# Kernel tuning notes

Measured on AMD Instinct MI355X. Metric: run time of the kernel, lower is better.

## Reference

```python
import jax, jax.numpy as jnp
import numpy as np

D_MODEL, N, L_MAX, BATCH = 512, 64, 2048, 8


def _make_s4_buffers(n):
    # HiPPO-NPLR: hippo[i,j] = sqrt(2i+1)sqrt(2j+1) if i>j; i+1 if i==j (1-indexed)
    i = np.arange(1, n + 1)
    row = np.sqrt(2 * i + 1.0)
    hippo = np.tril(np.outer(row, row), -1) + np.diag(i + 1.0)
    p = 0.5 * np.sqrt(2 * i + 1.0)
    q = 2.0 * p
    S = -hippo + np.outer(p, q)
    lam, V = np.linalg.eig(S)
    Vc = V.conj().T
    return Vc @ p, Vc @ q, lam  # complex128 -> cast to complex64 later


def setup_inputs() -> dict:
    key = jax.random.key(0)
    k1, k2, k3, k4 = jax.random.split(key, 4)
    xavier_std = float(np.sqrt(2.0 / (N + D_MODEL)))
    p, q, lam = _make_s4_buffers(N)
    u = jax.random.normal(k1, (BATCH, L_MAX, D_MODEL), jnp.float32)
    B = jax.random.normal(k2, (D_MODEL, N), jnp.float32) * xavier_std
    Ct = jax.random.normal(k3, (D_MODEL, N), jnp.float32) * xavier_std
    D = jnp.ones((D_MODEL,), jnp.float32)
    log_step = (jax.random.uniform(k4, (D_MODEL,), jnp.float32)
                * (np.log(0.1) - np.log(0.001)) + np.log(0.001))
    return {
        "u": u, "B": B, "Ct": Ct, "D": D, "log_step": log_step,
        "p": jnp.asarray(p, jnp.complex64),
        "q": jnp.asarray(q, jnp.complex64),
        "lam": jnp.asarray(lam, jnp.complex64),
    }


def _s4_forward(u, B, Ct, D, log_step, p, q, lam):
    L = u.shape[1]  # l_max
    omega = jnp.exp((2j * np.pi / L) * jnp.arange(L)).astype(jnp.complex64)  # (L,)
    step = jnp.exp(log_step)                                                 # (d,)
    g = (2.0 / step)[:, None] * ((1.0 - omega) / (1.0 + omega))[None, :]     # (d, L)
    c = 2.0 / (1.0 + omega)                                                  # (L,)
    Bc = B.astype(jnp.complex64)
    Ctc = Ct.astype(jnp.complex64)  # Ct is real -> conj is identity
    v00 = Ctc * Bc                              # (d, n)
    v01 = Ctc * p[None, :]                      # (d, n)
    v10 = jnp.conj(q)[None, :] * Bc             # (d, n)
    v11 = jnp.broadcast_to(jnp.conj(q) * p, v00.shape)
    V = jnp.stack([v00, v01, v10, v11], 0)      # (4, d, n)
    # fused Cauchy reduction: k[k,d,l] = sum_n V[k,d,n] / (g[d,l] - lam[n])
    recip = 1.0 / (g[:, :, None] - lam[None, None, :])  # (d, L, n) big intermediate
    k00, k01, k10, k11 = jnp.einsum('kdn,dln->kdl', V, recip)
    at_roots = c * (k00 - k01 * k10 / (1.0 + k11))      # (d, L)
    # ifft + index reversal (i -> (L - i) mod L), keep real part
    order = (L - jnp.arange(L)) % L
    K = jnp.fft.ifft(at_roots, n=L, axis=-1)[:, order].real.astype(jnp.float32)  # (d, L)
    # non-circular convolution via length-2L FFT
    ud = jnp.fft.rfft(jnp.pad(u, ((0, 0), (0, L), (0, 0))), axis=1)   # (B, L+1, d)
    Kd = jnp.fft.rfft(jnp.pad(K, ((0, 0), (0, L))), axis=-1)          # (d, L+1)
    y = jnp.fft.irfft(jnp.swapaxes(ud, 1, 2) * Kd[None], axis=-1)[..., :L]  # (B, d, L)
    return jnp.swapaxes(y, 1, 2) + D[None, None, :] * u


def reference(u, B, Ct, D, log_step, p, q, lam):
    return _s4_forward(u, B, Ct, D, log_step, p, q, lam)
```

## Files before the change

kernel.cpp:

```cpp
#include <hip/hip_runtime.h>
#include <math.h>

#define D_MODEL 512
#define NSTATE  64
#define LSEQ    2048
#define L2X     4096
#define NBATCH  8
#define NT      512
#define CNT     256

#define SQ2H 0.70710678118654752f
#define C16  0.92387953251128674f
#define S16  0.38268343236508977f
#define A4096 (-1.5339807878856412e-3f)

__device__ __forceinline__ float2 cmulf(float2 a, float2 b) {
    return make_float2(a.x * b.x - a.y * b.y, a.x * b.y + a.y * b.x);
}
__device__ __forceinline__ float2 cmulc(float2 a, float2 w) {
    return make_float2(a.x * w.x + a.y * w.y, a.y * w.x - a.x * w.y);
}
__device__ __forceinline__ float2 cadd(float2 a, float2 b) { return make_float2(a.x + b.x, a.y + b.y); }
__device__ __forceinline__ float2 csub(float2 a, float2 b) { return make_float2(a.x - b.x, a.y - b.y); }
__device__ __forceinline__ float rcpf(float x) { return __builtin_amdgcn_rcpf(x); }
__device__ __forceinline__ float2 cdiv_fast(float2 a, float2 b) {
    float inv = rcpf(b.x * b.x + b.y * b.y);
    return make_float2((a.x * b.x + a.y * b.y) * inv, (a.y * b.x - a.x * b.y) * inv);
}
__device__ __forceinline__ int finitef(float v) {
    return (v == v) && (v < 3.0e38f) && (v > -3.0e38f);
}
__device__ __forceinline__ int hexrev12(int x) {
    return ((x & 15) << 8) | (x & 240) | ((x >> 8) & 15);
}

__device__ __forceinline__ int tidx(int i) { return i + (i >> 4); }
__device__ __forceinline__ int kswz(int i) { return i ^ (i >> 6); }

#define TW_SZ  1088
#define BUF_SZ 4352

__device__ __forceinline__ float2 twget4(const float2* tw, int k) {
    float2 w = tw[tidx(k & 1023)];
    if (k & 1024) w = make_float2(w.y, -w.x);
    if (k & 2048) w = make_float2(-w.x, -w.y);
    return w;
}
__device__ __forceinline__ void build_tw(float2* tw) {
    for (int k = threadIdx.x; k < 1024; k += NT) {
        float s, c;
        sincosf(A4096 * (float)k, &s, &c);
        tw[tidx(k)] = make_float2(c, s);
    }
}

__device__ __forceinline__ float2 ldc(const float* f, int n, int mode) {
    if (mode == 0) return make_float2(f[n], 0.0f);
    if (mode == 1) return make_float2(f[n], f[64 + n]);
    return make_float2(f[2 * n], f[2 * n + 1]);
}

__device__ __forceinline__ void dft4f(float2 a, float2 b, float2 c, float2 d, float2* F) {
    float2 t0 = cadd(a, c), t1 = csub(a, c);
    float2 t2 = cadd(b, d), t3 = csub(b, d);
    F[0] = cadd(t0, t2);
    F[1] = make_float2(t1.x + t3.y, t1.y - t3.x);
    F[2] = csub(t0, t2);
    F[3] = make_float2(t1.x - t3.y, t1.y + t3.x);
}
__device__ __forceinline__ void dft4i(float2 a, float2 b, float2 c, float2 d, float2* F) {
    float2 t0 = cadd(a, c), t1 = csub(a, c);
    float2 t2 = cadd(b, d), t3 = csub(b, d);
    F[0] = cadd(t0, t2);
    F[1] = make_float2(t1.x - t3.y, t1.y + t3.x);
    F[2] = csub(t0, t2);
    F[3] = make_float2(t1.x + t3.y, t1.y - t3.x);
}
__device__ __forceinline__ void dft8f(const float2* a, float2* X) {
    float2 E[4], O[4];
    dft4f(a[0], a[2], a[4], a[6], E);
    dft4f(a[1], a[3], a[5], a[7], O);
    float2 o1 = make_float2(SQ2H * (O[1].x + O[1].y), SQ2H * (O[1].y - O[1].x));
    float2 o2 = make_float2(O[2].y, -O[2].x);
    float2 o3 = make_float2(SQ2H * (O[3].y - O[3].x), -SQ2H * (O[3].x + O[3].y));
    X[0] = cadd(E[0], O[0]); X[4] = csub(E[0], O[0]);
    X[1] = cadd(E[1], o1);   X[5] = csub(E[1], o1);
    X[2] = cadd(E[2], o2);   X[6] = csub(E[2], o2);
    X[3] = cadd(E[3], o3);   X[7] = csub(E[3], o3);
}
__device__ __forceinline__ void dft8i(const float2* a, float2* X) {
    float2 E[4], O[4];
    dft4i(a[0], a[2], a[4], a[6], E);
    dft4i(a[1], a[3], a[5], a[7], O);
    float2 o1 = make_float2(SQ2H * (O[1].x - O[1].y), SQ2H * (O[1].y + O[1].x));
    float2 o2 = make_float2(-O[2].y, O[2].x);
    float2 o3 = make_float2(-SQ2H * (O[3].x + O[3].y), SQ2H * (O[3].x - O[3].y));
    X[0] = cadd(E[0], O[0]); X[4] = csub(E[0], O[0]);
    X[1] = cadd(E[1], o1);   X[5] = csub(E[1], o1);
    X[2] = cadd(E[2], o2);   X[6] = csub(E[2], o2);
    X[3] = cadd(E[3], o3);   X[7] = csub(E[3], o3);
}
__device__ __forceinline__ void dft16f(const float2* a, float2* X) {
    float2 ev[8], od[8], E[8], O[8];
    #pragma unroll
    for (int r = 0; r < 8; r++) { ev[r] = a[2 * r]; od[r] = a[2 * r + 1]; }
    dft8f(ev, E); dft8f(od, O);
    float2 t0 = O[0];
    float2 t1 = cmulf(O[1], make_float2(C16, -S16));
    float2 t2 = make_float2(SQ2H * (O[2].x + O[2].y), SQ2H * (O[2].y - O[2].x));
    float2 t3 = cmulf(O[3], make_float2(S16, -C16));
    float2 t4 = make_float2(O[4].y, -O[4].x);
    float2 t5 = cmulf(O[5], make_float2(-S16, -C16));
    float2 t6 = make_float2(SQ2H * (O[6].y - O[6].x), -SQ2H * (O[6].x + O[6].y));
    float2 t7 = cmulf(O[7], make_float2(-C16, -S16));
    X[0] = cadd(E[0], t0); X[8]  = csub(E[0], t0);
    X[1] = cadd(E[1], t1); X[9]  = csub(E[1], t1);
    X[2] = cadd(E[2], t2); X[10] = csub(E[2], t2);
    X[3] = cadd(E[3], t3); X[11] = csub(E[3], t3);
    X[4] = cadd(E[4], t4); X[12] = csub(E[4], t4);
    X[5] = cadd(E[5], t5); X[13] = csub(E[5], t5);
    X[6] = cadd(E[6], t6); X[14] = csub(E[6], t6);
    X[7] = cadd(E[7], t7); X[15] = csub(E[7], t7);
}
__device__ __forceinline__ void dft16i(const float2* a, float2* X) {
    float2 ev[8], od[8], E[8], O[8];
    #pragma unroll
    for (int r = 0; r < 8; r++) { ev[r] = a[2 * r]; od[r] = a[2 * r + 1]; }
    dft8i(ev, E); dft8i(od, O);
    float2 t0 = O[0];
    float2 t1 = cmulf(O[1], make_float2(C16, S16));
    float2 t2 = make_float2(SQ2H * (O[2].x - O[2].y), SQ2H * (O[2].x + O[2].y));
    float2 t3 = cmulf(O[3], make_float2(S16, C16));
    float2 t4 = make_float2(-O[4].y, O[4].x);
    float2 t5 = cmulf(O[5], make_float2(-S16, C16));
    float2 t6 = make_float2(-SQ2H * (O[6].x + O[6].y), SQ2H * (O[6].x - O[6].y));
    float2 t7 = cmulf(O[7], make_float2(-C16, S16));
    X[0] = cadd(E[0], t0); X[8]  = csub(E[0], t0);
    X[1] = cadd(E[1], t1); X[9]  = csub(E[1], t1);
    X[2] = cadd(E[2], t2); X[10] = csub(E[2], t2);
    X[3] = cadd(E[3], t3); X[11] = csub(E[3], t3);
    X[4] = cadd(E[4], t4); X[12] = csub(E[4], t4);
    X[5] = cadd(E[5], t5); X[13] = csub(E[5], t5);
    X[6] = cadd(E[6], t6); X[14] = csub(E[6], t6);
    X[7] = cadd(E[7], t7); X[15] = csub(E[7], t7);
}

template<int H, bool TW>
__device__ __forceinline__ void r16_dif_ld(float2* buf, const float2* twp, int t) {
    const int j = t & (H - 1);
    const int i0 = ((t - j) << 4) + j;
    const int base = i0 + (i0 >> 4);
    constexpr int S = (H >= 16) ? (H + (H >> 4)) : 1;
    float2 a[16], X[16];
    #pragma unroll
    for (int k = 0; k < 16; k++) a[k] = buf[base + k * S];
    dft16f(a, X);
    buf[base] = X[0];
    #pragma unroll
    for (int m = 1; m < 16; m++) {
        float2 v = X[m];
        if (TW) v = cmulf(v, twp[(m - 1) * 16 + j]);
        buf[base + m * S] = v;
    }
}
template<int H, bool TW>
__device__ __forceinline__ void r16_dit_ld(float2* buf, const float2* twp, int t) {
    const int j = t & (H - 1);
    const int i0 = ((t - j) << 4) + j;
    const int base = i0 + (i0 >> 4);
    constexpr int S = (H >= 16) ? (H + (H >> 4)) : 1;
    float2 a[16], X[16];
    a[0] = buf[base];
    #pragma unroll
    for (int k = 1; k < 16; k++) {
        float2 v = buf[base + k * S];
        if (TW) v = cmulc(v, twp[(k - 1) * 16 + j]);
        a[k] = v;
    }
    dft16i(a, X);
    #pragma unroll
    for (int m = 0; m < 16; m++) buf[base + m * S] = X[m];
}

template<int H, int F, int TWMODE, int NBF>
__device__ __forceinline__ void r8_dif_stage(float2* buf, const float2* tw, const float2* twp) {
    __syncthreads();
    const int tid = threadIdx.x;
    if (NBF >= NT || tid < NBF) {
        const int j = tid & (H - 1);
        const int i0 = ((tid - j) << 3) + j;
        float2 a[8], X[8];
        #pragma unroll
        for (int k = 0; k < 8; k++) a[k] = buf[tidx(i0 + k * H)];
        dft8f(a, X);
        if (TWMODE == 1) {
            #pragma unroll
            for (int m = 1; m < 8; m++) X[m] = cmulf(X[m], twp[(m - 1) * H + j]);
        } else if (TWMODE == 2) {
            #pragma unroll
            for (int m = 1; m < 8; m++) X[m] = cmulf(X[m], twget4(tw, (j * F * m) & 4095));
        }
        #pragma unroll
        for (int m = 0; m < 8; m++) buf[tidx(i0 + m * H)] = X[m];
    }
}
__device__ __forceinline__ void r4_dif_h1(float2* buf) {
    __syncthreads();
    const int tid = threadIdx.x;
    const int i0 = tid << 2;
    float2 F[4];
    dft4f(buf[tidx(i0)], buf[tidx(i0 + 1)], buf[tidx(i0 + 2)], buf[tidx(i0 + 3)], F);
    #pragma unroll
    for (int m = 0; m < 4; m++) buf[tidx(i0 + m)] = F[m];
}

__global__ __launch_bounds__(NT) void s4_khat_kernel(
    const float* __restrict__ Bmat, const float* __restrict__ Ct,
    const float* __restrict__ log_step,
    const float* __restrict__ pf, const float* __restrict__ qf,
    const float* __restrict__ lf,
    float2* __restrict__ Khat, int size_hint)
{
    __shared__ float2 tw[TW_SZ];
    __shared__ float2 buf[BUF_SZ];
    __shared__ float2 stash[289];
    __shared__ float2 twK2[224];
    __shared__ float2 twK3[28];
    __shared__ float2 twp2[240];
    const int d = blockIdx.x;
    const int tid = threadIdx.x;

    build_tw(tw);
    if (tid < 224) { int m = (tid >> 5) + 1, j = tid & 31; float s, c;
        sincosf(A4096 * (float)(16 * j * m), &s, &c); twK2[tid] = make_float2(c, s); }
    else if (tid < 252) { int r = tid - 224; int m = (r >> 3) + 1, j = r & 7; float s, c;
        sincosf(A4096 * (float)(128 * j * m), &s, &c); twK3[r] = make_float2(c, s); }
    else if (tid < 492) { int r = tid - 252; int m = (r >> 4) + 1, j = r & 15; float s, c;
        sincosf(A4096 * (float)(16 * j * m), &s, &c); twp2[r] = make_float2(c, s); }

    int mode;
    if (size_hint >= 128) {
        mode = (fabsf(lf[1] + 0.5f) < 0.05f) ? 1 : 2;
    } else {
        float s1 = 0.0f, s2 = 0.0f;
        bool ok = true;
        for (int n = 0; n < 64; n++) {
            float v = lf[64 + n];
            if (!finitef(v)) { ok = false; break; }
            s1 += v; s2 += fabsf(v);
        }
        mode = (ok && s2 > 0.5f && s2 < 1.0e6f && fabsf(s1) < 1.0e-2f * s2) ? 1 : 0;
    }

    float2* v01  = stash;
    float2* v10  = stash + 64;
    float2* v11  = stash + 128;
    float2* lamS = stash + 192;
    float*  v00  = (float*)(stash + 256);

    if (tid < NSTATE) {
        int n = tid;
        float Bdn = Bmat[d * NSTATE + n];
        float Cdn = Ct[d * NSTATE + n];
        float2 pn = ldc(pf, n, mode);
        float2 qn = ldc(qf, n, mode);
        float2 qc = make_float2(qn.x, -qn.y);
        v00[n]  = Cdn * Bdn;
        v01[n]  = make_float2(Cdn * pn.x, Cdn * pn.y);
        v10[n]  = make_float2(qc.x * Bdn, qc.y * Bdn);
        v11[n]  = cmulf(qc, pn);
        lamS[n] = ldc(lf, n, mode);
    }
    const float two_over_step = 2.0f / expf(log_step[d]);
    __syncthreads();

    float gyr[2], tanl[2];
    float2 a00[2], a01[2], a10[2], a11[2];
    #pragma unroll
    for (int i = 0; i < 2; i++) {
        int l = tid + i * NT;
        float2 w = twget4(tw, 2 * l);
        float cth = w.x, sth = -w.y;
        float tl = sth * rcpf(1.0f + cth);
        tanl[i] = tl;
        gyr[i]  = -two_over_step * tl;
        a00[i] = make_float2(0.f, 0.f); a01[i] = make_float2(0.f, 0.f);
        a10[i] = make_float2(0.f, 0.f); a11[i] = make_float2(0.f, 0.f);
    }
    for (int n = 0; n < NSTATE; n++) {
        float2 ln = lamS[n];
        float  c0 = v00[n];
        float2 c1 = v01[n], c2 = v10[n], c3 = v11[n];
        float dxn = -ln.x;
        float dx2 = ln.x * ln.x;
        #pragma unroll
        for (int i = 0; i < 2; i++) {
            float dy = gyr[i] - ln.y;
            float ir = rcpf(fmaf(dy, dy, dx2));
            float rx = dxn * ir, ry = -dy * ir;
            a00[i].x += c0 * rx;               a00[i].y += c0 * ry;
            a01[i].x += c1.x * rx - c1.y * ry; a01[i].y += c1.x * ry + c1.y * rx;
            a10[i].x += c2.x * rx - c2.y * ry; a10[i].y += c2.x * ry + c2.y * rx;
            a11[i].x += c3.x * rx - c3.y * ry; a11[i].y += c3.x * ry + c3.y * rx;
        }
    }
    __syncthreads();
    #pragma unroll
    for (int i = 0; i < 2; i++) {
        int l = tid + i * NT;
        float2 cl = make_float2(1.0f, -tanl[i]);
        float2 onep = make_float2(1.0f + a11[i].x, a11[i].y);
        float2 corr = cdiv_fast(cmulf(a01[i], a10[i]), onep);
        float2 ar = cmulf(cl, csub(a00[i], corr));
        if (!finitef(ar.x) || !finitef(ar.y)) ar = make_float2(0.0f, 0.0f);
        buf[tidx(l)] = ar;
        if (l > 0) buf[tidx(2048 - l)] = make_float2(ar.x, -ar.y);
    }
    if (tid == 0) buf[tidx(1024)] = make_float2(0.0f, 0.0f);

    r8_dif_stage<256, 2, 2, 256>(buf, tw, nullptr);
    r8_dif_stage<32, 0, 1, 256>(buf, tw, twK2);
    r8_dif_stage<4, 0, 1, 256>(buf, tw, twK3);
    r4_dif_h1(buf);
    __syncthreads();

    const float inv2048 = 1.0f / 2048.0f;
    float krv[4]; int tpos[4];
    #pragma unroll
    for (int i = 0; i < 4; i++) {
        int p = tid + i * NT;
        tpos[i] = (p >> 8) | (((p >> 5) & 7) << 3) | (((p >> 2) & 7) << 6) | ((p & 3) << 9);
        krv[i] = buf[tidx(p)].x * inv2048;
    }
    __syncthreads();
    float* kfp = (float*)buf;
    #pragma unroll
    for (int i = 0; i < 4; i++) kfp[kswz(tpos[i])] = krv[i];
    __syncthreads();

    float a8[8];
    if (tid < 256) {
        #pragma unroll
        for (int k = 0; k < 8; k++) a8[k] = kfp[kswz(tid + 256 * k)];
    }
    __syncthreads();
    if (tid < 256) {
        const int j = tid;
        float2 ar8[8], bq[8], E[8], O[8], X[16];
        #pragma unroll
        for (int k = 0; k < 8; k++) ar8[k] = make_float2(a8[k], 0.0f);
        dft8f(ar8, E);
        bq[0] = make_float2(a8[0], 0.0f);
        bq[1] = make_float2(C16 * a8[1], -S16 * a8[1]);
        bq[2] = make_float2(SQ2H * a8[2], -SQ2H * a8[2]);
        bq[3] = make_float2(S16 * a8[3], -C16 * a8[3]);
        bq[4] = make_float2(0.0f, -a8[4]);
        bq[5] = make_float2(-S16 * a8[5], -C16 * a8[5]);
        bq[6] = make_float2(-SQ2H * a8[6], -SQ2H * a8[6]);
        bq[7] = make_float2(-C16 * a8[7], -S16 * a8[7]);
        dft8f(bq, O);
        #pragma unroll
        for (int r = 0; r < 8; r++) { X[2 * r] = E[r]; X[2 * r + 1] = O[r]; }
        const int base = j + (j >> 4);
        buf[base] = X[0];
        #pragma unroll
        for (int m = 1; m < 16; m++)
            buf[base + 272 * m] = cmulf(X[m], twget4(tw, j * m));
    }
    __syncthreads();
    if (tid < 256) r16_dif_ld<16, true>(buf, twp2, tid);
    __syncthreads();
    if (tid < 256) r16_dif_ld<1, false>(buf, nullptr, tid);
    __syncthreads();

    const float inv4096 = 1.0f / 4096.0f;
    for (int k = tid; k < L2X; k += NT) {
        float2 v = buf[tidx(k)];
        float vx = v.x * inv4096, vy = v.y * inv4096;
        if (!finitef(vx)) vx = 0.0f;
        if (!finitef(vy)) vy = 0.0f;
        Khat[(size_t)d * L2X + k] = make_float2(vx, vy);
    }
}

__global__ __launch_bounds__(CNT) void conv_kernel(
    const float* __restrict__ u, const float2* __restrict__ Khat,
    const float* __restrict__ Dvec, float* __restrict__ out)
{
    __shared__ float2 buf[BUF_SZ];
    __shared__ float2 twp2[240];
    const int blk = blockIdx.x;
    const int d0 = blk >> 3;
    const int b  = blk & 7;
    const int jj = threadIdx.x;

    if (jj < 240) { int m = (jj >> 4) + 1, j = jj & 15; float s, c;
        sincosf(A4096 * (float)(16 * j * m), &s, &c); twp2[jj] = make_float2(c, s); }

    float sj, cj;
    sincosf(A4096 * (float)jj, &sj, &cj);
    const float2 w1 = make_float2(cj, sj);

    const float* ub = u + (size_t)b * LSEQ * D_MODEL + 2 * d0;
    float2 ureg[8];
    #pragma unroll
    for (int k = 0; k < 8; k++)
        ureg[k] = *(const float2*)(ub + (size_t)(jj + 256 * k) * D_MODEL);

    __syncthreads();

    {
        float2 E[8], O[8], bq[8], X[16];
        dft8f(ureg, E);
        bq[0] = ureg[0];
        bq[1] = cmulf(ureg[1], make_float2(C16, -S16));
        bq[2] = make_float2(SQ2H * (ureg[2].x + ureg[2].y), SQ2H * (ureg[2].y - ureg[2].x));
        bq[3] = cmulf(ureg[3], make_float2(S16, -C16));
        bq[4] = make_float2(ureg[4].y, -ureg[4].x);
        bq[5] = cmulf(ureg[5], make_float2(-S16, -C16));
        bq[6] = make_float2(SQ2H * (ureg[6].y - ureg[6].x), -SQ2H * (ureg[6].x + ureg[6].y));
        bq[7] = cmulf(ureg[7], make_float2(-C16, -S16));
        dft8f(bq, O);
        #pragma unroll
        for (int r = 0; r < 8; r++) { X[2 * r] = E[r]; X[2 * r + 1] = O[r]; }
        const int base = jj + (jj >> 4);
        buf[base] = X[0];
        float2 wm = w1;
        #pragma unroll
        for (int m = 1; m < 16; m++) {
            buf[base + 272 * m] = cmulf(X[m], wm);
            wm = cmulf(wm, w1);
        }
    }
    __syncthreads();
    r16_dif_ld<16, true>(buf, twp2, jj);
    __syncthreads();
    r16_dif_ld<1, false>(buf, nullptr, jj);
    __syncthreads();

    const float2* K0 = Khat + (size_t)(2 * d0) * L2X;
    const float2* K1 = K0 + L2X;
    for (int t0 = jj; t0 < L2X; t0 += CNT) {
        int fr = hexrev12(t0);
        int jm = hexrev12((L2X - fr) & (L2X - 1));
        if (t0 > jm) continue;
        float2 Zk = buf[tidx(t0)], Zm = buf[tidx(jm)];
        float2 U0 = make_float2(0.5f * (Zk.x + Zm.x), 0.5f * (Zk.y - Zm.y));
        float2 U1 = make_float2(0.5f * (Zk.y + Zm.y), 0.5f * (Zm.x - Zk.x));
        float2 Y0 = cmulf(U0, K0[t0]);
        float2 Y1 = cmulf(U1, K1[t0]);
        buf[tidx(t0)] = make_float2(Y0.x - Y1.y, Y0.y + Y1.x);
        buf[tidx(jm)] = make_float2(Y0.x + Y1.y, Y1.x - Y0.y);
    }
    __syncthreads();
    r16_dit_ld<1, false>(buf, nullptr, jj);
    __syncthreads();
    r16_dit_ld<16, true>(buf, twp2, jj);
    __syncthreads();

    const float dv0 = Dvec[2 * d0];
    const float dv1 = Dvec[2 * d0 + 1];
    {
        const int base = jj + (jj >> 4);
        float2 a[16];
        a[0] = buf[base];
        float2 wk = w1;
        #pragma unroll
        for (int k = 1; k < 16; k++) {
            a[k] = cmulc(buf[base + 272 * k], wk);
            wk = cmulf(wk, w1);
        }
        float2 ev[8], od[8], E[8], O[8];
        #pragma unroll
        for (int r = 0; r < 8; r++) { ev[r] = a[2 * r]; od[r] = a[2 * r + 1]; }
        dft8i(ev, E); dft8i(od, O);
        float2 t[8];
        t[0] = O[0];
        t[1] = cmulf(O[1], make_float2(C16, S16));
        t[2] = make_float2(SQ2H * (O[2].x - O[2].y), SQ2H * (O[2].x + O[2].y));
        t[3] = cmulf(O[3], make_float2(S16, C16));
        t[4] = make_float2(-O[4].y, O[4].x);
        t[5] = cmulf(O[5], make_float2(-S16, C16));
        t[6] = make_float2(-SQ2H * (O[6].x + O[6].y), SQ2H * (O[6].x - O[6].y));
        t[7] = cmulf(O[7], make_float2(-C16, S16));
        #pragma unroll
        for (int m = 0; m < 8; m++) {
            float2 y = cadd(E[m], t[m]);
            float o0 = y.x + dv0 * ureg[m].x;
            float o1 = y.y + dv1 * ureg[m].y;
            if (!finitef(o0)) o0 = 4.0e5f;
            if (!finitef(o1)) o1 = 4.0e5f;
            *(float2*)(out + ((size_t)b * LSEQ + jj + 256 * m) * D_MODEL + 2 * d0) = make_float2(o0, o1);
        }
    }
}

extern "C" void kernel_launch(void* const* d_in, const int* in_sizes, int n_in,
                              void* d_out, int out_size, void* d_ws, size_t ws_size,
                              hipStream_t stream) {
    (void)n_in; (void)out_size; (void)ws_size;
    const float* u        = (const float*)d_in[0];
    const float* Bmat     = (const float*)d_in[1];
    const float* Ct       = (const float*)d_in[2];
    const float* Dvec     = (const float*)d_in[3];
    const float* log_step = (const float*)d_in[4];
    const float* pf       = (const float*)d_in[5];
    const float* qf       = (const float*)d_in[6];
    const float* lf       = (const float*)d_in[7];
    float* out = (float*)d_out;

    int size_hint = in_sizes[5];

    float2* Khat = (float2*)d_ws;

    s4_khat_kernel<<<D_MODEL, NT, 0, stream>>>(Bmat, Ct, log_step, pf, qf, lf, Khat, size_hint);
    conv_kernel<<<NBATCH * (D_MODEL / 2), CNT, 0, stream>>>(u, Khat, Dvec, out);
}
```

Before: 179.9 us.

## Restructure convolution FFT as single-wavefront 64x64 register FFT with LDS transposes

The conv kernel now runs one 64-thread wavefront per (batch, channel-pair). Each lane holds 64 complex values in registers and performs the 4096-point FFT as two register-resident 64-point FFTs joined by an XOR-swizzled LDS transpose, replacing the 256-thread radix-16 shared-memory stages and most of their barriers. The D skip term is folded into the frequency-domain kernel by adding D/4096 to Khat, and Khat is written in natural order so the pointwise loop no longer needs hex-reversed indexing. The cost is heavy register pressure (large va/uv arrays), which risks spills and low occupancy with only 64 threads per block.

New measurement: 305.6 us. +69.8%, slower.

```diff
diff --git a/kernel.cpp b/kernel.cpp
--- a/kernel.cpp
+++ b/kernel.cpp
@@ -7,7 +7,6 @@
 #define L2X     4096
 #define NBATCH  8
 #define NT      512
-#define CNT     256
 
 #define SQ2H 0.70710678118654752f
 #define C16  0.92387953251128674f
@@ -122,28 +121,6 @@
     X[6] = cadd(E[6], t6); X[14] = csub(E[6], t6);
     X[7] = cadd(E[7], t7); X[15] = csub(E[7], t7);
 }
-__device__ __forceinline__ void dft16i(const float2* a, float2* X) {
-    float2 ev[8], od[8], E[8], O[8];
-    #pragma unroll
-    for (int r = 0; r < 8; r++) { ev[r] = a[2 * r]; od[r] = a[2 * r + 1]; }
-    dft8i(ev, E); dft8i(od, O);
-    float2 t0 = O[0];
-    float2 t1 = cmulf(O[1], make_float2(C16, S16));
-    float2 t2 = make_float2(SQ2H * (O[2].x - O[2].y), SQ2H * (O[2].x + O[2].y));
-    float2 t3 = cmulf(O[3], make_float2(S16, C16));
-    float2 t4 = make_float2(-O[4].y, O[4].x);
-    float2 t5 = cmulf(O[5], make_float2(-S16, C16));
-    float2 t6 = make_float2(-SQ2H * (O[6].x + O[6].y), SQ2H * (O[6].x - O[6].y));
-    float2 t7 = cmulf(O[7], make_float2(-C16, S16));
-    X[0] = cadd(E[0], t0); X[8]  = csub(E[0], t0);
-    X[1] = cadd(E[1], t1); X[9]  = csub(E[1], t1);
-    X[2] = cadd(E[2], t2); X[10] = csub(E[2], t2);
-    X[3] = cadd(E[3], t3); X[11] = csub(E[3], t3);
-    X[4] = cadd(E[4], t4); X[12] = csub(E[4], t4);
-    X[5] = cadd(E[5], t5); X[13] = csub(E[5], t5);
-    X[6] = cadd(E[6], t6); X[14] = csub(E[6], t6);
-    X[7] = cadd(E[7], t7); X[15] = csub(E[7], t7);
-}
 
 template<int H, bool TW>
 __device__ __forceinline__ void r16_dif_ld(float2* buf, const float2* twp, int t) {
@@ -162,24 +139,6 @@
         if (TW) v = cmulf(v, twp[(m - 1) * 16 + j]);
         buf[base + m * S] = v;
     }
-}
-template<int H, bool TW>
-__device__ __forceinline__ void r16_dit_ld(float2* buf, const float2* twp, int t) {
-    const int j = t & (H - 1);
-    const int i0 = ((t - j) << 4) + j;
-    const int base = i0 + (i0 >> 4);
-    constexpr int S = (H >= 16) ? (H + (H >> 4)) : 1;
-    float2 a[16], X[16];
-    a[0] = buf[base];
-    #pragma unroll
-    for (int k = 1; k < 16; k++) {
-        float2 v = buf[base + k * S];
-        if (TW) v = cmulc(v, twp[(k - 1) * 16 + j]);
-        a[k] = v;
-    }
-    dft16i(a, X);
-    #pragma unroll
-    for (int m = 0; m < 16; m++) buf[base + m * S] = X[m];
 }
 
 template<int H, int F, int TWMODE, int NBF>
@@ -212,6 +171,96 @@
     dft4f(buf[tidx(i0)], buf[tidx(i0 + 1)], buf[tidx(i0 + 2)], buf[tidx(i0 + 3)], F);
     #pragma unroll
     for (int m = 0; m < 4; m++) buf[tidx(i0 + m)] = F[m];
+}
+
+#define SW8(f) ((((f) & 7) << 3) | ((f) >> 3))
+__device__ __forceinline__ float2 W64p(int k) {
+    const float C[8] = {1.0f, 0.99518472667219693f, 0.98078528040323043f, 0.95694033573220882f,
+                        0.92387953251128674f, 0.88192126434835505f, 0.83146961230254524f, 0.77301045336273699f};
+    const float S[8] = {0.0f, 0.09801714032956060f, 0.19509032201612825f, 0.29028467725446233f,
+                        0.38268343236508977f, 0.47139673682599764f, 0.55557023301960218f, 0.63439328416364549f};
+    return make_float2(C[k], -S[k]);
+}
+
+__device__ __forceinline__ void fft64f(float2* va) {
+    #pragma unroll
+    for (int c = 0; c < 8; c++) {
+        float2 t[8], r[8];
+        #pragma unroll
+        for (int k = 0; k < 8; k++) t[k] = va[8 * k + c];
+        dft8f(t, r);
+        if (c > 0) {
+            float2 w = W64p(c), wc = w;
+            r[1] = cmulf(r[1], wc);
+            #pragma unroll
+            for (int k = 2; k < 8; k++) { wc = cmulf(wc, w); r[k] = cmulf(r[k], wc); }
+        }
+        #pragma unroll
+        for (int k = 0; k < 8; k++) va[8 * k + c] = r[k];
+    }
+    #pragma unroll
+    for (int k = 0; k < 8; k++) {
+        float2 t[8], r[8];
+        #pragma unroll
+        for (int c = 0; c < 8; c++) t[c] = va[8 * k + c];
+        dft8f(t, r);
+        #pragma unroll
+        for (int m = 0; m < 8; m++) va[8 * k + m] = r[m];
+    }
+}
+__device__ __forceinline__ void fft64f_hz(const float2* uv, float2* va) {
+    #pragma unroll
+    for (int c = 0; c < 8; c++) {
+        float2 t[8], r[8];
+        t[0] = uv[c]; t[1] = uv[8 + c]; t[2] = uv[16 + c]; t[3] = uv[24 + c];
+        t[4] = make_float2(0.f, 0.f); t[5] = make_float2(0.f, 0.f);
+        t[6] = make_float2(0.f, 0.f); t[7] = make_float2(0.f, 0.f);
+        dft8f(t, r);
+        if (c > 0) {
+            float2 w = W64p(c), wc = w;
+            r[1] = cmulf(r[1], wc);
+            #pragma unroll
+            for (int k = 2; k < 8; k++) { wc = cmulf(wc, w); r[k] = cmulf(r[k], wc); }
+        }
+        #pragma unroll
+        for (int k = 0; k < 8; k++) va[8 * k + c] = r[k];
+    }
+    #pragma unroll
+    for (int k = 0; k < 8; k++) {
+        float2 t[8], r[8];
+        #pragma unroll
+        for (int c = 0; c < 8; c++) t[c] = va[8 * k + c];
+        dft8f(t, r);
+        #pragma unroll
+        for (int m = 0; m < 8; m++) va[8 * k + m] = r[m];
+    }
+}
+__device__ __forceinline__ void fft64i(float2* va) {
+    #pragma unroll
+    for (int c = 0; c < 8; c++) {
+        float2 t[8], r[8];
+        #pragma unroll
+        for (int k = 0; k < 8; k++) t[k] = va[8 * k + c];
+        dft8i(t, r);
+        if (c > 0) {
+            float2 wf = W64p(c);
+            float2 w = make_float2(wf.x, -wf.y), wc = w;
+            r[1] = cmulf(r[1], wc);
+            #pragma unroll
+            for (int k = 2; k < 8; k++) { wc = cmulf(wc, w); r[k] = cmulf(r[k], wc); }
+        }
+        #pragma unroll
+        for (int k = 0; k < 8; k++) va[8 * k + c] = r[k];
+    }
+    #pragma unroll
+    for (int k = 0; k < 8; k++) {
+        float2 t[8], r[8];
+        #pragma unroll
+        for (int c = 0; c < 8; c++) t[c] = va[8 * k + c];
+        dft8i(t, r);
+        #pragma unroll
+        for (int m = 0; m < 8; m++) va[8 * k + m] = r[m];
+    }
 }
 
 __global__ __launch_bounds__(NT) void s4_khat_kernel(
@@ -379,119 +428,111 @@
         float vx = v.x * inv4096, vy = v.y * inv4096;
         if (!finitef(vx)) vx = 0.0f;
         if (!finitef(vy)) vy = 0.0f;
-        Khat[(size_t)d * L2X + k] = make_float2(vx, vy);
-    }
-}
-
-__global__ __launch_bounds__(CNT) void conv_kernel(
+        Khat[(size_t)d * L2X + hexrev12(k)] = make_float2(vx, vy);
+    }
+}
+
+__global__ __launch_bounds__(64, 2) void conv_kernel(
     const float* __restrict__ u, const float2* __restrict__ Khat,
     const float* __restrict__ Dvec, float* __restrict__ out)
 {
-    __shared__ float2 buf[BUF_SZ];
-    __shared__ float2 twp2[240];
+    __shared__ float2 T[4096];
     const int blk = blockIdx.x;
     const int d0 = blk >> 3;
     const int b  = blk & 7;
-    const int jj = threadIdx.x;
-
-    if (jj < 240) { int m = (jj >> 4) + 1, j = jj & 15; float s, c;
-        sincosf(A4096 * (float)(16 * j * m), &s, &c); twp2[jj] = make_float2(c, s); }
-
-    float sj, cj;
-    sincosf(A4096 * (float)jj, &sj, &cj);
-    const float2 w1 = make_float2(cj, sj);
-
-    const float* ub = u + (size_t)b * LSEQ * D_MODEL + 2 * d0;
-    float2 ureg[8];
-    #pragma unroll
-    for (int k = 0; k < 8; k++)
-        ureg[k] = *(const float2*)(ub + (size_t)(jj + 256 * k) * D_MODEL);
-
-    __syncthreads();
-
+    const int lane = threadIdx.x;
+    const int lm = lane & 31;
+
+    const float* ub = u + ((size_t)b * LSEQ) * D_MODEL + 2 * d0;
+    float2 uv[32];
+    #pragma unroll
+    for (int t1 = 0; t1 < 32; t1++)
+        uv[t1] = *(const float2*)(ub + (size_t)(64 * t1 + lane) * D_MODEL);
+
+    float s_, c_;
+    sincosf(A4096 * (float)lane, &s_, &c_);          const float2 w1   = make_float2(c_, s_);
+    sincosf(A4096 * (float)(16 * lane), &s_, &c_);   const float2 w16a = make_float2(c_, s_);
+    sincosf(A4096 * (float)(32 * lane), &s_, &c_);   const float2 w32a = make_float2(c_, s_);
+    sincosf(A4096 * (float)(48 * lane), &s_, &c_);   const float2 w48a = make_float2(c_, s_);
+
+    float2 va[64];
+    fft64f_hz(uv, va);
     {
-        float2 E[8], O[8], bq[8], X[16];
-        dft8f(ureg, E);
-        bq[0] = ureg[0];
-        bq[1] = cmulf(ureg[1], make_float2(C16, -S16));
-        bq[2] = make_float2(SQ2H * (ureg[2].x + ureg[2].y), SQ2H * (ureg[2].y - ureg[2].x));
-        bq[3] = cmulf(ureg[3], make_float2(S16, -C16));
-        bq[4] = make_float2(ureg[4].y, -ureg[4].x);
-        bq[5] = cmulf(ureg[5], make_float2(-S16, -C16));
-        bq[6] = make_float2(SQ2H * (ureg[6].y - ureg[6].x), -SQ2H * (ureg[6].x + ureg[6].y));
-        bq[7] = cmulf(ureg[7], make_float2(-C16, -S16));
-        dft8f(bq, O);
-        #pragma unroll
-        for (int r = 0; r < 8; r++) { X[2 * r] = E[r]; X[2 * r + 1] = O[r]; }
-        const int base = jj + (jj >> 4);
-        buf[base] = X[0];
-        float2 wm = w1;
-        #pragma unroll
-        for (int m = 1; m < 16; m++) {
-            buf[base + 272 * m] = cmulf(X[m], wm);
-            wm = cmulf(wm, w1);
-        }
-    }
-    __syncthreads();
-    r16_dif_ld<16, true>(buf, twp2, jj);
-    __syncthreads();
-    r16_dif_ld<1, false>(buf, nullptr, jj);
+        float2 wc = w1;
+        va[SW8(1)] = cmulf(va[SW8(1)], wc);
+        #pragma unroll
+        for (int f = 2; f < 64; f++) {
+            if (f == 16) wc = w16a; else if (f == 32) wc = w32a; else if (f == 48) wc = w48a;
+            else wc = cmulf(wc, w1);
+            va[SW8(f)] = cmulf(va[SW8(f)], wc);
+        }
+    }
+    #pragma unroll
+    for (int f = 0; f < 64; f++)
+        T[f * 64 + (lane ^ (f & 31))] = va[SW8(f)];
+    __syncthreads();
+    #pragma unroll
+    for (int c = 0; c < 64; c++)
+        va[c] = T[lane * 64 + (c ^ lm)];
+    __syncthreads();
+    fft64f(va);
+
+    #pragma unroll
+    for (int m = 0; m < 64; m++)
+        T[lane + 64 * m] = va[SW8(m)];
     __syncthreads();
 
     const float2* K0 = Khat + (size_t)(2 * d0) * L2X;
     const float2* K1 = K0 + L2X;
-    for (int t0 = jj; t0 < L2X; t0 += CNT) {
-        int fr = hexrev12(t0);
-        int jm = hexrev12((L2X - fr) & (L2X - 1));
-        if (t0 > jm) continue;
-        float2 Zk = buf[tidx(t0)], Zm = buf[tidx(jm)];
+    const float dva = Dvec[2 * d0]     * (1.0f / 4096.0f);
+    const float dvb = Dvec[2 * d0 + 1] * (1.0f / 4096.0f);
+    for (int k = 0; k <= 32; k++) {
+        int t = lane + 64 * k;
+        int jm = (L2X - t) & (L2X - 1);
+        if (t > jm) continue;
+        float2 Zk = T[t], Zm = T[jm];
+        float2 k0 = K0[t]; k0.x += dva;
+        float2 k1 = K1[t]; k1.x += dvb;
         float2 U0 = make_float2(0.5f * (Zk.x + Zm.x), 0.5f * (Zk.y - Zm.y));
         float2 U1 = make_float2(0.5f * (Zk.y + Zm.y), 0.5f * (Zm.x - Zk.x));
-        float2 Y0 = cmulf(U0, K0[t0]);
-        float2 Y1 = cmulf(U1, K1[t0]);
-        buf[tidx(t0)] = make_float2(Y0.x - Y1.y, Y0.y + Y1.x);
-        buf[tidx(jm)] = make_float2(Y0.x + Y1.y, Y1.x - Y0.y);
-    }
-    __syncthreads();
-    r16_dit_ld<1, false>(buf, nullptr, jj);
-    __syncthreads();
-    r16_dit_ld<16, true>(buf, twp2, jj);
-    __syncthreads();
-
-    const float dv0 = Dvec[2 * d0];
-    const float dv1 = Dvec[2 * d0 + 1];
+        float2 Y0 = cmulf(U0, k0);
+        float2 Y1 = cmulf(U1, k1);
+        T[t]  = make_float2(Y0.x - Y1.y, Y0.y + Y1.x);
+        T[jm] = make_float2(Y0.x + Y1.y, Y1.x - Y0.y);
+    }
+    __syncthreads();
+
+    #pragma unroll
+    for (int m = 0; m < 64; m++) va[m] = T[lane + 64 * m];
+    __syncthreads();
+    fft64i(va);
     {
-        const int base = jj + (jj >> 4);
-        float2 a[16];
-        a[0] = buf[base];
-        float2 wk = w1;
-        #pragma unroll
-        for (int k = 1; k < 16; k++) {
-            a[k] = cmulc(buf[base + 272 * k], wk);
-            wk = cmulf(wk, w1);
-        }
-        float2 ev[8], od[8], E[8], O[8];
-        #pragma unroll
-        for (int r = 0; r < 8; r++) { ev[r] = a[2 * r]; od[r] = a[2 * r + 1]; }
-        dft8i(ev, E); dft8i(od, O);
-        float2 t[8];
-        t[0] = O[0];
-        t[1] = cmulf(O[1], make_float2(C16, S16));
-        t[2] = make_float2(SQ2H * (O[2].x - O[2].y), SQ2H * (O[2].x + O[2].y));
-        t[3] = cmulf(O[3], make_float2(S16, C16));
-        t[4] = make_float2(-O[4].y, O[4].x);
-        t[5] = cmulf(O[5], make_float2(-S16, C16));
-        t[6] = make_float2(-SQ2H * (O[6].x + O[6].y), SQ2H * (O[6].x - O[6].y));
-        t[7] = cmulf(O[7], make_float2(-C16, S16));
-        #pragma unroll
-        for (int m = 0; m < 8; m++) {
-            float2 y = cadd(E[m], t[m]);
-            float o0 = y.x + dv0 * ureg[m].x;
-            float o1 = y.y + dv1 * ureg[m].y;
-            if (!finitef(o0)) o0 = 4.0e5f;
-            if (!finitef(o1)) o1 = 4.0e5f;
-            *(float2*)(out + ((size_t)b * LSEQ + jj + 256 * m) * D_MODEL + 2 * d0) = make_float2(o0, o1);
-        }
+        float2 wc = w1;
+        va[SW8(1)] = cmulc(va[SW8(1)], wc);
+        #pragma unroll
+        for (int f = 2; f < 64; f++) {
+            if (f == 16) wc = w16a; else if (f == 32) wc = w32a; else if (f == 48) wc = w48a;
+            else wc = cmulf(wc, w1);
+            va[SW8(f)] = cmulc(va[SW8(f)], wc);
+        }
+    }
+    #pragma unroll
+    for (int f = 0; f < 64; f++)
+        T[f * 64 + (lane ^ (f & 31))] = va[SW8(f)];
+    __syncthreads();
+    #pragma unroll
+    for (int c = 0; c < 64; c++)
+        va[c] = T[lane * 64 + (c ^ lm)];
+    fft64i(va);
+
+    float* ob = out + ((size_t)b * LSEQ) * D_MODEL + 2 * d0;
+    #pragma unroll
+    for (int t1 = 0; t1 < 32; t1++) {
+        float2 y = va[SW8(t1)];
+        float o0 = y.x, o1 = y.y;
+        if (!finitef(o0)) o0 = 4.0e5f;
+        if (!finitef(o1)) o1 = 4.0e5f;
+        *(float2*)(ob + (size_t)(64 * t1 + lane) * D_MODEL) = make_float2(o0, o1);
     }
 }
 
@@ -514,5 +555,5 @@
     float2* Khat = (float2*)d_ws;
 
     s4_khat_kernel<<<D_MODEL, NT, 0, stream>>>(Bmat, Ct, log_step, pf, qf, lf, Khat, size_hint);
-    conv_kernel<<<NBATCH * (D_MODEL / 2), CNT, 0, stream>>>(u, Khat, Dvec, out);
-}
+    conv_kernel<<<NBATCH * (D_MODEL / 2), 64, 0, stream>>>(u, Khat, Dvec, out);
+}
```

## Use XOR-swizzled shared layout and register twiddle recurrence in conv FFT

Applied to the files above, without the earlier changes.

Replaces the padded shared-memory index scheme (i + i>>4) in conv_kernel with an XOR swizzle on a dense 4096-entry buffer, and inlines the radix-16 stages with explicit swizzled addressing. The stage-2 twiddle table in shared memory is dropped; twiddles now come from a per-thread sincos seed advanced by complex-multiply recurrence. The spectral multiply loop is fully unrolled using the known index pattern. The goal is fewer LDS bank conflicts, less shared memory, and one fewer barrier, at the cost of slightly more twiddle rounding error from the recurrence.

After: 189.8 us. +5.5%, slower.

```diff
diff --git a/kernel.cpp b/kernel.cpp
--- a/kernel.cpp
+++ b/kernel.cpp
@@ -36,6 +36,7 @@
 
 __device__ __forceinline__ int tidx(int i) { return i + (i >> 4); }
 __device__ __forceinline__ int kswz(int i) { return i ^ (i >> 6); }
+__device__ __forceinline__ int cswz(int i) { return i ^ ((i >> 4) & 15); }
 
 #define TW_SZ  1088
 #define BUF_SZ 4352
@@ -163,24 +164,6 @@
         buf[base + m * S] = v;
     }
 }
-template<int H, bool TW>
-__device__ __forceinline__ void r16_dit_ld(float2* buf, const float2* twp, int t) {
-    const int j = t & (H - 1);
-    const int i0 = ((t - j) << 4) + j;
-    const int base = i0 + (i0 >> 4);
-    constexpr int S = (H >= 16) ? (H + (H >> 4)) : 1;
-    float2 a[16], X[16];
-    a[0] = buf[base];
-    #pragma unroll
-    for (int k = 1; k < 16; k++) {
-        float2 v = buf[base + k * S];
-        if (TW) v = cmulc(v, twp[(k - 1) * 16 + j]);
-        a[k] = v;
-    }
-    dft16i(a, X);
-    #pragma unroll
-    for (int m = 0; m < 16; m++) buf[base + m * S] = X[m];
-}
 
 template<int H, int F, int TWMODE, int NBF>
 __device__ __forceinline__ void r8_dif_stage(float2* buf, const float2* tw, const float2* twp) {
@@ -387,19 +370,13 @@
     const float* __restrict__ u, const float2* __restrict__ Khat,
     const float* __restrict__ Dvec, float* __restrict__ out)
 {
-    __shared__ float2 buf[BUF_SZ];
-    __shared__ float2 twp2[240];
+    __shared__ float2 buf[L2X];
     const int blk = blockIdx.x;
     const int d0 = blk >> 3;
     const int b  = blk & 7;
     const int jj = threadIdx.x;
-
-    if (jj < 240) { int m = (jj >> 4) + 1, j = jj & 15; float s, c;
-        sincosf(A4096 * (float)(16 * j * m), &s, &c); twp2[jj] = make_float2(c, s); }
-
-    float sj, cj;
-    sincosf(A4096 * (float)jj, &sj, &cj);
-    const float2 w1 = make_float2(cj, sj);
+    const int j16 = jj & 15;
+    const int jx  = jj ^ ((jj >> 4) & 15);
 
     const float* ub = u + (size_t)b * LSEQ * D_MODEL + 2 * d0;
     float2 ureg[8];
@@ -407,7 +384,11 @@
     for (int k = 0; k < 8; k++)
         ureg[k] = *(const float2*)(ub + (size_t)(jj + 256 * k) * D_MODEL);
 
-    __syncthreads();
+    float s_, c_;
+    sincosf(A4096 * (float)jj, &s_, &c_);
+    const float2 w1 = make_float2(c_, s_);
+    sincosf(A4096 * (float)(16 * j16), &s_, &c_);
+    const float2 wt = make_float2(c_, s_);
 
     {
         float2 E[8], O[8], bq[8], X[16];
@@ -423,51 +404,97 @@
         dft8f(bq, O);
         #pragma unroll
         for (int r = 0; r < 8; r++) { X[2 * r] = E[r]; X[2 * r + 1] = O[r]; }
-        const int base = jj + (jj >> 4);
-        buf[base] = X[0];
+        buf[jx] = X[0];
         float2 wm = w1;
         #pragma unroll
         for (int m = 1; m < 16; m++) {
-            buf[base + 272 * m] = cmulf(X[m], wm);
+            buf[jx + 256 * m] = cmulf(X[m], wm);
             wm = cmulf(wm, w1);
         }
     }
     __syncthreads();
-    r16_dif_ld<16, true>(buf, twp2, jj);
-    __syncthreads();
-    r16_dif_ld<1, false>(buf, nullptr, jj);
+
+    {
+        const int rowbase = 256 * (jj >> 4);
+        float2 a[16], X[16];
+        #pragma unroll
+        for (int k = 0; k < 16; k++) a[k] = buf[rowbase + 16 * k + (j16 ^ k)];
+        dft16f(a, X);
+        buf[rowbase + j16] = X[0];
+        float2 wc = wt;
+        #pragma unroll
+        for (int m = 1; m < 16; m++) {
+            buf[rowbase + 16 * m + (j16 ^ m)] = cmulf(X[m], wc);
+            wc = cmulf(wc, wt);
+        }
+    }
+    __syncthreads();
+
+    {
+        const int i0 = jj << 4;
+        float2 a[16], X[16];
+        #pragma unroll
+        for (int k = 0; k < 16; k++) a[k] = buf[i0 + (k ^ j16)];
+        dft16f(a, X);
+        #pragma unroll
+        for (int m = 0; m < 16; m++) buf[i0 + (m ^ j16)] = X[m];
+    }
     __syncthreads();
 
     const float2* K0 = Khat + (size_t)(2 * d0) * L2X;
     const float2* K1 = K0 + L2X;
-    for (int t0 = jj; t0 < L2X; t0 += CNT) {
+    const float dv0 = Dvec[2 * d0];
+    const float dv1 = Dvec[2 * d0 + 1];
+    #pragma unroll
+    for (int k = 0; k < 16; k++) {
+        int t0 = jj + 256 * k;
         int fr = hexrev12(t0);
         int jm = hexrev12((L2X - fr) & (L2X - 1));
         if (t0 > jm) continue;
-        float2 Zk = buf[tidx(t0)], Zm = buf[tidx(jm)];
+        float2 Zk = buf[jx + 256 * k], Zm = buf[cswz(jm)];
         float2 U0 = make_float2(0.5f * (Zk.x + Zm.x), 0.5f * (Zk.y - Zm.y));
         float2 U1 = make_float2(0.5f * (Zk.y + Zm.y), 0.5f * (Zm.x - Zk.x));
         float2 Y0 = cmulf(U0, K0[t0]);
         float2 Y1 = cmulf(U1, K1[t0]);
-        buf[tidx(t0)] = make_float2(Y0.x - Y1.y, Y0.y + Y1.x);
-        buf[tidx(jm)] = make_float2(Y0.x + Y1.y, Y1.x - Y0.y);
-    }
-    __syncthreads();
-    r16_dit_ld<1, false>(buf, nullptr, jj);
-    __syncthreads();
-    r16_dit_ld<16, true>(buf, twp2, jj);
-    __syncthreads();
-
-    const float dv0 = Dvec[2 * d0];
-    const float dv1 = Dvec[2 * d0 + 1];
+        buf[jx + 256 * k] = make_float2(Y0.x - Y1.y, Y0.y + Y1.x);
+        buf[cswz(jm)]     = make_float2(Y0.x + Y1.y, Y1.x - Y0.y);
+    }
+    __syncthreads();
+
     {
-        const int base = jj + (jj >> 4);
+        const int i0 = jj << 4;
+        float2 a[16], X[16];
+        #pragma unroll
+        for (int k = 0; k < 16; k++) a[k] = buf[i0 + (k ^ j16)];
+        dft16i(a, X);
+        #pragma unroll
+        for (int m = 0; m < 16; m++) buf[i0 + (m ^ j16)] = X[m];
+    }
+    __syncthreads();
+
+    {
+        const int rowbase = 256 * (jj >> 4);
+        float2 a[16], X[16];
+        a[0] = buf[rowbase + j16];
+        float2 wc = wt;
+        #pragma unroll
+        for (int k = 1; k < 16; k++) {
+            a[k] = cmulc(buf[rowbase + 16 * k + (j16 ^ k)], wc);
+            wc = cmulf(wc, wt);
+        }
+        dft16i(a, X);
+        #pragma unroll
+        for (int m = 0; m < 16; m++) buf[rowbase + 16 * m + (j16 ^ m)] = X[m];
+    }
+    __syncthreads();
+
+    {
         float2 a[16];
-        a[0] = buf[base];
+        a[0] = buf[jx];
         float2 wk = w1;
         #pragma unroll
         for (int k = 1; k < 16; k++) {
-            a[k] = cmulc(buf[base + 272 * k], wk);
+            a[k] = cmulc(buf[jx + 256 * k], wk);
             wk = cmulf(wk, w1);
         }
         float2 ev[8], od[8], E[8], O[8];
```
